# Performance work log

Hardware: AMD Instinct MI355X
Metric: run time of the kernel (lower is better)

Reference implementation:

```python
import jax, jax.numpy as jnp
import numpy as np

B, S, DM, H, DK, R, THETA = 8, 2048, 512, 8, 64, 128, 10000.0
BLK = R          # key/query block size; window radius == block size
NB = S // BLK    # number of blocks
NEG = -1e30      # additive mask for invalid positions (fp32-safe)


def setup_inputs() -> dict:
    key = jax.random.key(0)
    ks = jax.random.split(key, 5)
    scale = 0.02
    hidden_states = jax.random.normal(ks[0], (B, S, DM), jnp.float32)
    Wq = jax.random.normal(ks[1], (DM, H * DK), jnp.float32) * scale
    Wk = jax.random.normal(ks[2], (DM, H * DK), jnp.float32) * scale
    Wv = jax.random.normal(ks[3], (DM, H * DK), jnp.float32) * scale
    Wo = jax.random.normal(ks[4], (H * DK, DM), jnp.float32) * scale
    position_ids = jnp.tile(jnp.arange(S, dtype=jnp.int64)[None, :], (B, 1))
    return {"hidden_states": hidden_states, "Wq": Wq, "Wk": Wk, "Wv": Wv,
            "Wo": Wo, "position_ids": position_ids}


def _apply_rope(q, k, position_ids):
    # q,k: [B,H,S,DK]; position_ids: [B,S]
    half = DK // 2
    inv_freq = 1.0 / (THETA ** (jnp.arange(0, DK, 2, dtype=jnp.float32) / DK))  # [half]
    freqs = position_ids.astype(jnp.float32)[:, :, None] * inv_freq[None, None, :]  # [B,S,half]
    emb = jnp.concatenate([freqs, freqs], axis=-1)        # [B,S,DK]
    cos = jnp.cos(emb)[:, None, :, :]                     # [B,1,S,DK]
    sin = jnp.sin(emb)[:, None, :, :]

    def rotate_half(x):
        return jnp.concatenate([-x[..., half:], x[..., :half]], axis=-1)

    return q * cos + rotate_half(q) * sin, k * cos + rotate_half(k) * sin


def _band_mask():
    # valid[nb, BLK, 3*BLK]: key within [0,S) and |j - i| <= R
    b = jnp.arange(NB)[:, None, None]
    qi = jnp.arange(BLK)[None, :, None]
    kj = jnp.arange(3 * BLK)[None, None, :]
    kglob = (b - 1) * BLK + kj                 # global key index
    qglob = b * BLK + qi                        # global query index
    return (jnp.abs(kglob - qglob) <= R) & (kglob >= 0) & (kglob < S)


def reference(hidden_states, Wq, Wk, Wv, Wo, position_ids):
    # projections: [B,S,DM] -> [B,H,S,DK]
    def shape(x):
        return x.reshape(B, S, H, DK).transpose(0, 2, 1, 3)

    q = shape(hidden_states @ Wq)
    k = shape(hidden_states @ Wk)
    v = shape(hidden_states @ Wv)
    q, k = _apply_rope(q, k, position_ids)

    # block-banded sliding-window attention, softmax_scale = 1.0 (no scaling)
    pad = ((0, 0), (0, 0), (BLK, BLK), (0, 0))
    kb = jnp.pad(k, pad).reshape(B, H, NB + 2, BLK, DK)
    vb = jnp.pad(v, pad).reshape(B, H, NB + 2, BLK, DK)
    # neighbor window: blocks [b-1, b, b+1] -> [B,H,NB,3*BLK,DK]
    kwin = jnp.concatenate([kb[:, :, i:i + NB] for i in range(3)], axis=3)
    vwin = jnp.concatenate([vb[:, :, i:i + NB] for i in range(3)], axis=3)
    qb = q.reshape(B, H, NB, BLK, DK)

    scores = jnp.einsum('bhnqd,bhnkd->bhnqk', qb, kwin)   # unscaled
    valid = _band_mask()                                  # [NB,BLK,3*BLK]
    scores = jnp.where(valid[None, None], scores, NEG)
    attn = jax.nn.softmax(scores.astype(jnp.float32), axis=-1).astype(scores.dtype)
    outb = jnp.einsum('bhnqk,bhnkd->bhnqd', attn, vwin)   # [B,H,NB,BLK,DK]

    out = outb.reshape(B, H, S, DK).transpose(0, 2, 1, 3).reshape(B, S, H * DK)
    return out @ Wo
```

## Files before the change

kernel.cpp:

```cpp
#include <hip/hip_runtime.h>

using bf16 = __bf16;
typedef __bf16 bf16x8 __attribute__((ext_vector_type(8)));
typedef __bf16 bf16x4 __attribute__((ext_vector_type(4)));
typedef float f32x4 __attribute__((ext_vector_type(4)));
typedef float f32x16 __attribute__((ext_vector_type(16)));

#define MFMA16(a, b, c) __builtin_amdgcn_mfma_f32_16x16x32_bf16((a), (b), (c), 0, 0, 0)
#define MFMA32(a, b, c) __builtin_amdgcn_mfma_f32_32x32x16_bf16((a), (b), (c), 0, 0, 0)

constexpr int S = 2048, DM = 512, H = 8, DK = 64, HD = 512;
constexpr int NBLK = 16, BLK = 128;
constexpr int Mrows = 8 * S;
constexpr float LOG2E = 1.44269504088896340736f;

__device__ __forceinline__ void gll16(const void* g, void* l) {
  __builtin_amdgcn_global_load_lds((const __attribute__((address_space(1))) unsigned int*)g,
                                   (__attribute__((address_space(3))) unsigned int*)l, 16, 0, 0);
}

__global__ void k_conv(const float* __restrict__ x, bf16* __restrict__ y) {
  size_t i = ((size_t)blockIdx.x * 256 + threadIdx.x) * 8;
  float4 a = *(const float4*)(x + i);
  float4 b = *(const float4*)(x + i + 4);
  bf16x8 o;
  o[0] = (bf16)a.x; o[1] = (bf16)a.y; o[2] = (bf16)a.z; o[3] = (bf16)a.w;
  o[4] = (bf16)b.x; o[5] = (bf16)b.y; o[6] = (bf16)b.z; o[7] = (bf16)b.w;
  *(bf16x8*)(y + i) = o;
}

__global__ void k_transw4(const float* __restrict__ W0, const float* __restrict__ W1,
                          const float* __restrict__ W2, const float* __restrict__ W3,
                          bf16* __restrict__ D0, bf16* __restrict__ D1,
                          bf16* __restrict__ D2, bf16* __restrict__ D3) {
  const int z = blockIdx.z;
  const float* W = (z == 0) ? W0 : (z == 1) ? W1 : (z == 2) ? W2 : W3;
  bf16* Wt = (z == 0) ? D0 : (z == 1) ? D1 : (z == 2) ? D2 : D3;
  __shared__ float tile[32][33];
  int k0 = blockIdx.x * 32, n0 = blockIdx.y * 32;
  int tx = threadIdx.x, ty = threadIdx.y;
#pragma unroll
  for (int i = 0; i < 4; i++)
    tile[ty * 4 + i][tx] = W[(size_t)(k0 + ty * 4 + i) * 512 + n0 + tx];
  __syncthreads();
#pragma unroll
  for (int i = 0; i < 4; i++)
    Wt[(size_t)(n0 + ty * 4 + i) * 512 + k0 + tx] = (bf16)tile[tx][ty * 4 + i];
}

__global__ void k_ctab(float2* __restrict__ ctab) {
  int idx = blockIdx.x * 256 + threadIdx.x;
  int s = idx >> 5, i = idx & 31;
  float invf = exp2f(-(float)i * (13.287712379549449f / 32.0f));
  float ang = (float)s * invf;
  ctab[idx] = make_float2(cosf(ang), sinf(ang));
}

__global__ __launch_bounds__(256) void k_gemm_qkv(
    const bf16* __restrict__ Xb,
    const bf16* __restrict__ Wtq, const bf16* __restrict__ Wtk, const bf16* __restrict__ Wtv,
    bf16* __restrict__ Qo, bf16* __restrict__ Ko, bf16* __restrict__ Vt,
    const float2* __restrict__ ctab) {
  const int bid = blockIdx.x;
  const int xcd = bid & 7, i = bid >> 3;
  const int mloc = i / 12, zy = i % 12;
  const int z = zy >> 2, y = zy & 3;
  const bf16* Wt = (z == 0) ? Wtq : ((z == 1) ? Wtk : Wtv);
  bf16* dst = (z == 0) ? Qo : Ko;
  const float qscale = (z == 0) ? LOG2E : 1.0f;

  __shared__ __align__(16) char Asm2[2][8192];
  __shared__ __align__(16) char Bsm2[2][8192];

  const int t = threadIdx.x, l = t & 63, wid = t >> 6;
  const int l15 = l & 15, l4 = l >> 4;
  const int wm = wid >> 1, wn = wid & 1;
  const size_t arow0 = (size_t)(xcd * 16 + mloc) * 128;
  const size_t brow0 = (size_t)y * 128;

  f32x4 acc[4][4] = {};
  const int rs = wid * 16 + (l >> 2);
  const int cs = (l & 3) ^ ((l >> 2) & 3);

  auto stage = [&](int kt, int b) {
    const int k0 = kt * 32;
    gll16(Xb + (arow0 + rs) * 512 + k0 + cs * 8,      Asm2[b] + wid * 1024);
    gll16(Xb + (arow0 + 64 + rs) * 512 + k0 + cs * 8, Asm2[b] + 4096 + wid * 1024);
    gll16(Wt + (brow0 + rs) * 512 + k0 + cs * 8,      Bsm2[b] + wid * 1024);
    gll16(Wt + (brow0 + 64 + rs) * 512 + k0 + cs * 8, Bsm2[b] + 4096 + wid * 1024);
  };

  stage(0, 0);
  asm volatile("s_waitcnt vmcnt(0)" ::: "memory");
  __builtin_amdgcn_s_barrier();

  int cur = 0;
  for (int kt = 0; kt < 16; ++kt) {
    if (kt < 15) stage(kt + 1, cur ^ 1);
    bf16x8 af[4], bfr[4];
#pragma unroll
    for (int mi = 0; mi < 4; mi++) {
      int row = wm * 64 + mi * 16 + l15;
      af[mi] = *(const bf16x8*)(Asm2[cur] + row * 64 + ((l4 ^ (row & 3)) * 16));
    }
#pragma unroll
    for (int ni = 0; ni < 4; ni++) {
      int row = wn * 64 + ni * 16 + l15;
      bfr[ni] = *(const bf16x8*)(Bsm2[cur] + row * 64 + ((l4 ^ (row & 3)) * 16));
    }
#pragma unroll
    for (int mi = 0; mi < 4; mi++)
#pragma unroll
      for (int ni = 0; ni < 4; ni++)
        acc[mi][ni] = MFMA16(af[mi], bfr[ni], acc[mi][ni]);
    if (kt < 15) {
      asm volatile("s_waitcnt vmcnt(0)" ::: "memory");
      __builtin_amdgcn_s_barrier();
    }
    cur ^= 1;
  }

  if (z == 2) {
    const int b = (int)(arow0 >> 11);
#pragma unroll
    for (int mi = 0; mi < 4; mi++) {
      int scol = (int)(arow0 & 2047) + wm * 64 + mi * 16 + l4 * 4;
#pragma unroll
      for (int ni = 0; ni < 4; ni++) {
        int col = (int)brow0 + wn * 64 + ni * 16 + l15;
        int hh = col >> 6, dd = col & 63;
        bf16x4 pk = {(bf16)acc[mi][ni][0], (bf16)acc[mi][ni][1],
                     (bf16)acc[mi][ni][2], (bf16)acc[mi][ni][3]};
        *(bf16x4*)(Vt + ((size_t)((b * H + hh) * 64 + dd)) * 2048 + scol) = pk;
      }
    }
    return;
  }

#pragma unroll
  for (int mi = 0; mi < 4; mi++) {
#pragma unroll
    for (int r = 0; r < 4; r++) {
      int grow = (int)arow0 + wm * 64 + mi * 16 + l4 * 4 + r;
      size_t rowoff = (size_t)grow * 512 + brow0 + wn * 64;
      int s = grow & (S - 1);
      float2 cs0 = ctab[s * 32 + l15];
      float2 cs1 = ctab[s * 32 + 16 + l15];
#pragma unroll
      for (int ni = 0; ni < 4; ni++) {
        float a = acc[mi][ni][r];
        float b = acc[mi][ni ^ 2][r];
        float2 cc = (ni & 1) ? cs1 : cs0;
        float val = (ni < 2) ? (a * cc.x - b * cc.y) : (a * cc.x + b * cc.y);
        dst[rowoff + ni * 16 + l15] = (bf16)(val * qscale);
      }
    }
  }
}

__global__ __launch_bounds__(256) void k_gemm_out(
    const bf16* __restrict__ A, const bf16* __restrict__ Wt, float* __restrict__ out) {
  const int bid = blockIdx.x;
  const int xcd = bid & 7, i = bid >> 3;
  __shared__ __align__(16) char Asm2[2][8192];
  __shared__ __align__(16) char Bsm2[2][8192];

  const int t = threadIdx.x, l = t & 63, wid = t >> 6;
  const int l15 = l & 15, l4 = l >> 4;
  const int wm = wid >> 1, wn = wid & 1;
  const size_t arow0 = (size_t)(xcd * 16 + (i >> 2)) * 128;
  const size_t brow0 = (size_t)(i & 3) * 128;

  f32x4 acc[4][4] = {};
  const int rs = wid * 16 + (l >> 2);
  const int cs = (l & 3) ^ ((l >> 2) & 3);

  auto stage = [&](int kt, int b) {
    const int k0 = kt * 32;
    gll16(A + (arow0 + rs) * 512 + k0 + cs * 8,       Asm2[b] + wid * 1024);
    gll16(A + (arow0 + 64 + rs) * 512 + k0 + cs * 8,  Asm2[b] + 4096 + wid * 1024);
    gll16(Wt + (brow0 + rs) * 512 + k0 + cs * 8,      Bsm2[b] + wid * 1024);
    gll16(Wt + (brow0 + 64 + rs) * 512 + k0 + cs * 8, Bsm2[b] + 4096 + wid * 1024);
  };

  stage(0, 0);
  asm volatile("s_waitcnt vmcnt(0)" ::: "memory");
  __builtin_amdgcn_s_barrier();

  int cur = 0;
  for (int kt = 0; kt < 16; ++kt) {
    if (kt < 15) stage(kt + 1, cur ^ 1);
    bf16x8 af[4], bfr[4];
#pragma unroll
    for (int mi = 0; mi < 4; mi++) {
      int row = wm * 64 + mi * 16 + l15;
      af[mi] = *(const bf16x8*)(Asm2[cur] + row * 64 + ((l4 ^ (row & 3)) * 16));
    }
#pragma unroll
    for (int ni = 0; ni < 4; ni++) {
      int row = wn * 64 + ni * 16 + l15;
      bfr[ni] = *(const bf16x8*)(Bsm2[cur] + row * 64 + ((l4 ^ (row & 3)) * 16));
    }
#pragma unroll
    for (int mi = 0; mi < 4; mi++)
#pragma unroll
      for (int ni = 0; ni < 4; ni++)
        acc[mi][ni] = MFMA16(af[mi], bfr[ni], acc[mi][ni]);
    if (kt < 15) {
      asm volatile("s_waitcnt vmcnt(0)" ::: "memory");
      __builtin_amdgcn_s_barrier();
    }
    cur ^= 1;
  }

#pragma unroll
  for (int mi = 0; mi < 4; mi++)
#pragma unroll
    for (int r = 0; r < 4; r++) {
      int grow = (int)arow0 + wm * 64 + mi * 16 + l4 * 4 + r;
      size_t rowoff = (size_t)grow * 512 + brow0 + wn * 64;
#pragma unroll
      for (int ni = 0; ni < 4; ni++)
        out[rowoff + ni * 16 + l15] = acc[mi][ni][r];
    }
}

__global__ __launch_bounds__(256, 4) void k_attn(
    const bf16* __restrict__ Q, const bf16* __restrict__ K, const bf16* __restrict__ Vt,
    bf16* __restrict__ O) {
  const int bid = blockIdx.x;
  const int swz = (bid & 7) * 128 + (bid >> 3);
  const int nb = swz & 15, h = (swz >> 4) & 7, bb = swz >> 7;
  const int t = threadIdx.x, l = t & 63, w = t >> 6;
  const int q31 = l & 31, hi = l >> 5;

  const int bh = bb * H + h;
  const size_t qrow = (size_t)bb * S + nb * BLK + w * 32 + q31;

  const bf16* Qp = Q + qrow * HD + h * DK + hi * 8;
  bf16x8 qb[4];
#pragma unroll
  for (int ks = 0; ks < 4; ks++) qb[ks] = *(const bf16x8*)(Qp + ks * 16);

  f32x16 o0 = {}, o1 = {};
  float mrun = -3e38f, lrun = 0.f;

  const bf16* Kbase = K + (size_t)bb * S * HD + h * DK + hi * 8;
  const bf16* Vbase = Vt + ((size_t)bh * 64 + q31) * 2048 + hi * 8;
  const int s0 = nb * BLK + w * 32 - 128;

  auto pv = [&](const f32x16& p, int kgc) {
    unsigned int Wd[4][2];
#pragma unroll
    for (int a = 0; a < 4; a++)
#pragma unroll
      for (int b2 = 0; b2 < 2; b2++) {
        unsigned int wd;
        asm("v_cvt_pk_bf16_f32 %0, %1, %2" : "=v"(wd) : "v"(p[4 * a + 2 * b2]), "v"(p[4 * a + 2 * b2 + 1]));
        Wd[a][b2] = wd;
      }
    bf16x8 pf[2];
#pragma unroll
    for (int ks = 0; ks < 2; ks++) {
      union { unsigned int u[4]; bf16x8 v; } cvt;
#pragma unroll
      for (int b2 = 0; b2 < 2; b2++) {
        unsigned int low_w = Wd[2 * ks][b2];
        unsigned int hi_w  = Wd[2 * ks + 1][b2];
        unsigned int msg = hi ? low_w : hi_w;
        unsigned int rec = __shfl_xor(msg, 32);
        cvt.u[b2]     = hi ? rec : low_w;
        cvt.u[2 + b2] = hi ? hi_w : rec;
      }
      pf[ks] = cvt.v;
    }
    const bf16* Vp = Vbase + kgc;
    o0 = MFMA32(*(const bf16x8*)(Vp), pf[0], o0);
    o0 = MFMA32(*(const bf16x8*)(Vp + 16), pf[1], o0);
    o1 = MFMA32(*(const bf16x8*)(Vp + 32 * 2048), pf[0], o1);
    o1 = MFMA32(*(const bf16x8*)(Vp + 32 * 2048 + 16), pf[1], o1);
  };

#pragma unroll
  for (int st = 0; st < 5; ++st) {
    const bool has2 = (st < 4);
    const int c0 = st * 2, c1 = c0 + 1;
    const int kg0 = s0 + c0 * 32, kg1 = s0 + c1 * 32;
    const int kc0 = kg0 < 0 ? 0 : (kg0 > S - 32 ? S - 32 : kg0);
    const int kc1 = kg1 < 0 ? 0 : (kg1 > S - 32 ? S - 32 : kg1);

    f32x16 a0 = {}, a1 = {};
    {
      const bf16* Kp = Kbase + (size_t)(kc0 + q31) * HD;
      a0 = MFMA32(*(const bf16x8*)(Kp),      qb[0], a0);
      a0 = MFMA32(*(const bf16x8*)(Kp + 16), qb[1], a0);
      a0 = MFMA32(*(const bf16x8*)(Kp + 32), qb[2], a0);
      a0 = MFMA32(*(const bf16x8*)(Kp + 48), qb[3], a0);
    }
    if (has2) {
      const bf16* Kp = Kbase + (size_t)(kc1 + q31) * HD;
      a1 = MFMA32(*(const bf16x8*)(Kp),      qb[0], a1);
      a1 = MFMA32(*(const bf16x8*)(Kp + 16), qb[1], a1);
      a1 = MFMA32(*(const bf16x8*)(Kp + 32), qb[2], a1);
      a1 = MFMA32(*(const bf16x8*)(Kp + 48), qb[3], a1);
    }

    if (kg0 != kc0) {
#pragma unroll
      for (int rg = 0; rg < 16; rg++) a0[rg] = -1e30f;
    } else if (c0 == 0) {
#pragma unroll
      for (int rg = 0; rg < 16; rg++) {
        int kk = (rg & 3) + 8 * (rg >> 2) + 4 * hi;
        if (kk < q31) a0[rg] = -1e30f;
      }
    } else if (c0 == 8) {
#pragma unroll
      for (int rg = 0; rg < 16; rg++) {
        int kk = (rg & 3) + 8 * (rg >> 2) + 4 * hi;
        if (kk > q31) a0[rg] = -1e30f;
      }
    }
    if (has2 && kg1 != kc1) {
#pragma unroll
      for (int rg = 0; rg < 16; rg++) a1[rg] = -1e30f;
    }

    f32x16 mx = a0;
    if (has2) {
#pragma unroll
      for (int rg = 0; rg < 16; rg++) mx[rg] = fmaxf(mx[rg], a1[rg]);
    }
#pragma unroll
    for (int sl = 8; sl >= 1; sl >>= 1)
#pragma unroll
      for (int i2 = 0; i2 < sl; i2++) mx[i2] = fmaxf(mx[i2], mx[i2 + sl]);
    const float pm = fmaxf(mx[0], __shfl_xor(mx[0], 32));

    if (!__all(pm - mrun <= 8.0f)) {
      const float mnew = fmaxf(mrun, pm);
      const float alpha = exp2f(mrun - mnew);
      lrun *= alpha;
#pragma unroll
      for (int rg = 0; rg < 16; rg++) { o0[rg] *= alpha; o1[rg] *= alpha; }
      mrun = mnew;
    }

    float rsum = 0.f;
#pragma unroll
    for (int rg = 0; rg < 16; rg++) { a0[rg] = exp2f(a0[rg] - mrun); rsum += a0[rg]; }
    if (has2) {
#pragma unroll
      for (int rg = 0; rg < 16; rg++) { a1[rg] = exp2f(a1[rg] - mrun); rsum += a1[rg]; }
    }
    rsum += __shfl_xor(rsum, 32);
    lrun += rsum;

    pv(a0, kc0);
    if (has2) pv(a1, kc1);
  }

  const float inv = 1.0f / lrun;
  bf16* Op = O + qrow * HD + h * DK + 4 * hi;
#pragma unroll
  for (int dt = 0; dt < 2; dt++) {
    const f32x16 oo = dt ? o1 : o0;
#pragma unroll
    for (int a = 0; a < 4; a++) {
      bf16x4 ob = {(bf16)(oo[4 * a + 0] * inv), (bf16)(oo[4 * a + 1] * inv),
                   (bf16)(oo[4 * a + 2] * inv), (bf16)(oo[4 * a + 3] * inv)};
      *(bf16x4*)(Op + dt * 32 + 8 * a) = ob;
    }
  }
}

extern "C" void kernel_launch(void* const* d_in, const int* in_sizes, int n_in,
                              void* d_out, int out_size, void* d_ws, size_t ws_size,
                              hipStream_t stream) {
  const float* hs = (const float*)d_in[0];
  const float* Wq = (const float*)d_in[1];
  const float* Wk = (const float*)d_in[2];
  const float* Wv = (const float*)d_in[3];
  const float* Wo = (const float*)d_in[4];
  float* out = (float*)d_out;

  char* ws = (char*)d_ws;
  const size_t MB = 1u << 20;
  bf16* Xb = (bf16*)(ws);
  bf16* Qb = (bf16*)(ws + 16 * MB);
  bf16* Kb = (bf16*)(ws + 32 * MB);
  bf16* Vt = (bf16*)(ws + 48 * MB);
  bf16* Wtq = (bf16*)(ws + 64 * MB);
  bf16* Wtk = Wtq + 512 * 512;
  bf16* Wtv = Wtk + 512 * 512;
  bf16* Wto = Wtv + 512 * 512;
  float2* ctab = (float2*)(ws + 64 * MB + 4 * 512 * 512 * sizeof(bf16));
  bf16* AO = Xb;

  k_conv<<<dim3(Mrows * DM / (256 * 8)), dim3(256), 0, stream>>>(hs, Xb);
  k_transw4<<<dim3(16, 16, 4), dim3(32, 8), 0, stream>>>(Wq, Wk, Wv, Wo, Wtq, Wtk, Wtv, Wto);
  k_ctab<<<dim3(S * 32 / 256), dim3(256), 0, stream>>>(ctab);
  k_gemm_qkv<<<dim3(1536), dim3(256), 0, stream>>>(Xb, Wtq, Wtk, Wtv, Qb, Kb, Vt, ctab);
  k_attn<<<dim3(NBLK * H * 8), dim3(256), 0, stream>>>(Qb, Kb, Vt, AO);
  k_gemm_out<<<dim3(512), dim3(256), 0, stream>>>(AO, Wto, out);
}
```

Baseline: 124.7 us.

## Software-pipeline K/V loads across single 32-key chunks in attention loop

Measured after the change: 126.1 us. About the same (+1.1%).

```diff
diff --git a/kernel.cpp b/kernel.cpp
--- a/kernel.cpp
+++ b/kernel.cpp
@@ -249,15 +249,88 @@
   const bf16* Vbase = Vt + ((size_t)bh * 64 + q31) * 2048 + hi * 8;
   const int s0 = nb * BLK + w * 32 - 128;
 
-  auto pv = [&](const f32x16& p, int kgc) {
+  auto kcl = [](int kg) { return kg < 0 ? 0 : (kg > S - 32 ? S - 32 : kg); };
+
+  bf16x8 kcur0, kcur1, kcur2, kcur3;
+  {
+    const bf16* Kp = Kbase + (size_t)(kcl(s0) + q31) * HD;
+    kcur0 = *(const bf16x8*)(Kp);
+    kcur1 = *(const bf16x8*)(Kp + 16);
+    kcur2 = *(const bf16x8*)(Kp + 32);
+    kcur3 = *(const bf16x8*)(Kp + 48);
+  }
+
+#pragma unroll
+  for (int c = 0; c < 9; ++c) {
+    const int kg = s0 + c * 32;
+    const int kcc = kcl(kg);
+    const int kcn = kcl(s0 + (c + 1) * 32);
+
+    const bf16* Vp = Vbase + kcc;
+    bf16x8 v0 = *(const bf16x8*)(Vp);
+    bf16x8 v1 = *(const bf16x8*)(Vp + 16);
+    bf16x8 v2 = *(const bf16x8*)(Vp + 32 * 2048);
+    bf16x8 v3 = *(const bf16x8*)(Vp + 32 * 2048 + 16);
+    const bf16* Kpn = Kbase + (size_t)(kcn + q31) * HD;
+    bf16x8 kn0 = *(const bf16x8*)(Kpn);
+    bf16x8 kn1 = *(const bf16x8*)(Kpn + 16);
+    bf16x8 kn2 = *(const bf16x8*)(Kpn + 32);
+    bf16x8 kn3 = *(const bf16x8*)(Kpn + 48);
+    __builtin_amdgcn_sched_barrier(0);
+
+    f32x16 a = {};
+    a = MFMA32(kcur0, qb[0], a);
+    a = MFMA32(kcur1, qb[1], a);
+    a = MFMA32(kcur2, qb[2], a);
+    a = MFMA32(kcur3, qb[3], a);
+
+    if (kg != kcc) {
+#pragma unroll
+      for (int rg = 0; rg < 16; rg++) a[rg] = -1e30f;
+    } else if (c == 0) {
+#pragma unroll
+      for (int rg = 0; rg < 16; rg++) {
+        int kk = (rg & 3) + 8 * (rg >> 2) + 4 * hi;
+        if (kk < q31) a[rg] = -1e30f;
+      }
+    } else if (c == 8) {
+#pragma unroll
+      for (int rg = 0; rg < 16; rg++) {
+        int kk = (rg & 3) + 8 * (rg >> 2) + 4 * hi;
+        if (kk > q31) a[rg] = -1e30f;
+      }
+    }
+
+    f32x16 mx = a;
+#pragma unroll
+    for (int sl = 8; sl >= 1; sl >>= 1)
+#pragma unroll
+      for (int i2 = 0; i2 < sl; i2++) mx[i2] = fmaxf(mx[i2], mx[i2 + sl]);
+    const float pm = fmaxf(mx[0], __shfl_xor(mx[0], 32));
+
+    if (!__all(pm - mrun <= 8.0f)) {
+      const float mnew = fmaxf(mrun, pm);
+      const float alpha = exp2f(mrun - mnew);
+      lrun *= alpha;
+#pragma unroll
+      for (int rg = 0; rg < 16; rg++) { o0[rg] *= alpha; o1[rg] *= alpha; }
+      mrun = mnew;
+    }
+
+    float rsum = 0.f;
+#pragma unroll
+    for (int rg = 0; rg < 16; rg++) { a[rg] = exp2f(a[rg] - mrun); rsum += a[rg]; }
+    rsum += __shfl_xor(rsum, 32);
+    lrun += rsum;
+
     unsigned int Wd[4][2];
 #pragma unroll
-    for (int a = 0; a < 4; a++)
+    for (int aa = 0; aa < 4; aa++)
 #pragma unroll
       for (int b2 = 0; b2 < 2; b2++) {
         unsigned int wd;
-        asm("v_cvt_pk_bf16_f32 %0, %1, %2" : "=v"(wd) : "v"(p[4 * a + 2 * b2]), "v"(p[4 * a + 2 * b2 + 1]));
-        Wd[a][b2] = wd;
+        asm("v_cvt_pk_bf16_f32 %0, %1, %2" : "=v"(wd) : "v"(a[4 * aa + 2 * b2]), "v"(a[4 * aa + 2 * b2 + 1]));
+        Wd[aa][b2] = wd;
       }
     bf16x8 pf[2];
 #pragma unroll
@@ -274,90 +347,13 @@
       }
       pf[ks] = cvt.v;
     }
-    const bf16* Vp = Vbase + kgc;
-    o0 = MFMA32(*(const bf16x8*)(Vp), pf[0], o0);
-    o0 = MFMA32(*(const bf16x8*)(Vp + 16), pf[1], o0);
-    o1 = MFMA32(*(const bf16x8*)(Vp + 32 * 2048), pf[0], o1);
-    o1 = MFMA32(*(const bf16x8*)(Vp + 32 * 2048 + 16), pf[1], o1);
-  };
-
-#pragma unroll
-  for (int st = 0; st < 5; ++st) {
-    const bool has2 = (st < 4);
-    const int c0 = st * 2, c1 = c0 + 1;
-    const int kg0 = s0 + c0 * 32, kg1 = s0 + c1 * 32;
-    const int kc0 = kg0 < 0 ? 0 : (kg0 > S - 32 ? S - 32 : kg0);
-    const int kc1 = kg1 < 0 ? 0 : (kg1 > S - 32 ? S - 32 : kg1);
-
-    f32x16 a0 = {}, a1 = {};
-    {
-      const bf16* Kp = Kbase + (size_t)(kc0 + q31) * HD;
-      a0 = MFMA32(*(const bf16x8*)(Kp),      qb[0], a0);
-      a0 = MFMA32(*(const bf16x8*)(Kp + 16), qb[1], a0);
-      a0 = MFMA32(*(const bf16x8*)(Kp + 32), qb[2], a0);
-      a0 = MFMA32(*(const bf16x8*)(Kp + 48), qb[3], a0);
-    }
-    if (has2) {
-      const bf16* Kp = Kbase + (size_t)(kc1 + q31) * HD;
-      a1 = MFMA32(*(const bf16x8*)(Kp),      qb[0], a1);
-      a1 = MFMA32(*(const bf16x8*)(Kp + 16), qb[1], a1);
-      a1 = MFMA32(*(const bf16x8*)(Kp + 32), qb[2], a1);
-      a1 = MFMA32(*(const bf16x8*)(Kp + 48), qb[3], a1);
-    }
-
-    if (kg0 != kc0) {
-#pragma unroll
-      for (int rg = 0; rg < 16; rg++) a0[rg] = -1e30f;
-    } else if (c0 == 0) {
-#pragma unroll
-      for (int rg = 0; rg < 16; rg++) {
-        int kk = (rg & 3) + 8 * (rg >> 2) + 4 * hi;
-        if (kk < q31) a0[rg] = -1e30f;
-      }
-    } else if (c0 == 8) {
-#pragma unroll
-      for (int rg = 0; rg < 16; rg++) {
-        int kk = (rg & 3) + 8 * (rg >> 2) + 4 * hi;
-        if (kk > q31) a0[rg] = -1e30f;
-      }
-    }
-    if (has2 && kg1 != kc1) {
-#pragma unroll
-      for (int rg = 0; rg < 16; rg++) a1[rg] = -1e30f;
-    }
-
-    f32x16 mx = a0;
-    if (has2) {
-#pragma unroll
-      for (int rg = 0; rg < 16; rg++) mx[rg] = fmaxf(mx[rg], a1[rg]);
-    }
-#pragma unroll
-    for (int sl = 8; sl >= 1; sl >>= 1)
-#pragma unroll
-      for (int i2 = 0; i2 < sl; i2++) mx[i2] = fmaxf(mx[i2], mx[i2 + sl]);
-    const float pm = fmaxf(mx[0], __shfl_xor(mx[0], 32));
-
-    if (!__all(pm - mrun <= 8.0f)) {
-      const float mnew = fmaxf(mrun, pm);
-      const float alpha = exp2f(mrun - mnew);
-      lrun *= alpha;
-#pragma unroll
-      for (int rg = 0; rg < 16; rg++) { o0[rg] *= alpha; o1[rg] *= alpha; }
-      mrun = mnew;
-    }
-
-    float rsum = 0.f;
-#pragma unroll
-    for (int rg = 0; rg < 16; rg++) { a0[rg] = exp2f(a0[rg] - mrun); rsum += a0[rg]; }
-    if (has2) {
-#pragma unroll
-      for (int rg = 0; rg < 16; rg++) { a1[rg] = exp2f(a1[rg] - mrun); rsum += a1[rg]; }
-    }
-    rsum += __shfl_xor(rsum, 32);
-    lrun += rsum;
-
-    pv(a0, kc0);
-    if (has2) pv(a1, kc1);
+
+    o0 = MFMA32(v0, pf[0], o0);
+    o0 = MFMA32(v1, pf[1], o0);
+    o1 = MFMA32(v2, pf[0], o1);
+    o1 = MFMA32(v3, pf[1], o1);
+
+    kcur0 = kn0; kcur1 = kn1; kcur2 = kn2; kcur3 = kn3;
   }
 
   const float inv = 1.0f / lrun;
@@ -366,10 +362,10 @@
   for (int dt = 0; dt < 2; dt++) {
     const f32x16 oo = dt ? o1 : o0;
 #pragma unroll
-    for (int a = 0; a < 4; a++) {
-      bf16x4 ob = {(bf16)(oo[4 * a + 0] * inv), (bf16)(oo[4 * a + 1] * inv),
-                   (bf16)(oo[4 * a + 2] * inv), (bf16)(oo[4 * a + 3] * inv)};
-      *(bf16x4*)(Op + dt * 32 + 8 * a) = ob;
+    for (int a2 = 0; a2 < 4; a2++) {
+      bf16x4 ob = {(bf16)(oo[4 * a2 + 0] * inv), (bf16)(oo[4 * a2 + 1] * inv),
+                   (bf16)(oo[4 * a2 + 2] * inv), (bf16)(oo[4 * a2 + 3] * inv)};
+      *(bf16x4*)(Op + dt * 32 + 8 * a2) = ob;
     }
   }
 }
```

## Triple-buffer GEMM LDS staging, change swizzle, and raise wave priority around attention MFMAs

Applied to the files above, without the earlier changes.

New measurement: 119.8 us. 3.9% less time.

```diff
diff --git a/kernel.cpp b/kernel.cpp
--- a/kernel.cpp
+++ b/kernel.cpp
@@ -69,8 +69,8 @@
   bf16* dst = (z == 0) ? Qo : Ko;
   const float qscale = (z == 0) ? LOG2E : 1.0f;
 
-  __shared__ __align__(16) char Asm2[2][8192];
-  __shared__ __align__(16) char Bsm2[2][8192];
+  __shared__ __align__(16) char Asm3[3][8192];
+  __shared__ __align__(16) char Bsm3[3][8192];
 
   const int t = threadIdx.x, l = t & 63, wid = t >> 6;
   const int l15 = l & 15, l4 = l >> 4;
@@ -80,33 +80,34 @@
 
   f32x4 acc[4][4] = {};
   const int rs = wid * 16 + (l >> 2);
-  const int cs = (l & 3) ^ ((l >> 2) & 3);
+  const int cs = (l & 3) ^ (l >> 4);
 
   auto stage = [&](int kt, int b) {
     const int k0 = kt * 32;
-    gll16(Xb + (arow0 + rs) * 512 + k0 + cs * 8,      Asm2[b] + wid * 1024);
-    gll16(Xb + (arow0 + 64 + rs) * 512 + k0 + cs * 8, Asm2[b] + 4096 + wid * 1024);
-    gll16(Wt + (brow0 + rs) * 512 + k0 + cs * 8,      Bsm2[b] + wid * 1024);
-    gll16(Wt + (brow0 + 64 + rs) * 512 + k0 + cs * 8, Bsm2[b] + 4096 + wid * 1024);
+    gll16(Xb + (arow0 + rs) * 512 + k0 + cs * 8,      Asm3[b] + wid * 1024);
+    gll16(Xb + (arow0 + 64 + rs) * 512 + k0 + cs * 8, Asm3[b] + 4096 + wid * 1024);
+    gll16(Wt + (brow0 + rs) * 512 + k0 + cs * 8,      Bsm3[b] + wid * 1024);
+    gll16(Wt + (brow0 + 64 + rs) * 512 + k0 + cs * 8, Bsm3[b] + 4096 + wid * 1024);
   };
 
   stage(0, 0);
-  asm volatile("s_waitcnt vmcnt(0)" ::: "memory");
+  stage(1, 1);
+  asm volatile("s_waitcnt vmcnt(4)" ::: "memory");
   __builtin_amdgcn_s_barrier();
 
   int cur = 0;
   for (int kt = 0; kt < 16; ++kt) {
-    if (kt < 15) stage(kt + 1, cur ^ 1);
+    if (kt + 2 <= 15) stage(kt + 2, (kt + 2) % 3);
     bf16x8 af[4], bfr[4];
 #pragma unroll
     for (int mi = 0; mi < 4; mi++) {
       int row = wm * 64 + mi * 16 + l15;
-      af[mi] = *(const bf16x8*)(Asm2[cur] + row * 64 + ((l4 ^ (row & 3)) * 16));
+      af[mi] = *(const bf16x8*)(Asm3[cur] + row * 64 + ((l4 ^ (l15 >> 2)) * 16));
     }
 #pragma unroll
     for (int ni = 0; ni < 4; ni++) {
       int row = wn * 64 + ni * 16 + l15;
-      bfr[ni] = *(const bf16x8*)(Bsm2[cur] + row * 64 + ((l4 ^ (row & 3)) * 16));
+      bfr[ni] = *(const bf16x8*)(Bsm3[cur] + row * 64 + ((l4 ^ (l15 >> 2)) * 16));
     }
 #pragma unroll
     for (int mi = 0; mi < 4; mi++)
@@ -114,10 +115,11 @@
       for (int ni = 0; ni < 4; ni++)
         acc[mi][ni] = MFMA16(af[mi], bfr[ni], acc[mi][ni]);
     if (kt < 15) {
-      asm volatile("s_waitcnt vmcnt(0)" ::: "memory");
+      if (kt < 14) asm volatile("s_waitcnt vmcnt(4)" ::: "memory");
+      else         asm volatile("s_waitcnt vmcnt(0)" ::: "memory");
       __builtin_amdgcn_s_barrier();
     }
-    cur ^= 1;
+    cur = (cur == 2) ? 0 : cur + 1;
   }
 
   if (z == 2) {
@@ -162,8 +164,8 @@
     const bf16* __restrict__ A, const bf16* __restrict__ Wt, float* __restrict__ out) {
   const int bid = blockIdx.x;
   const int xcd = bid & 7, i = bid >> 3;
-  __shared__ __align__(16) char Asm2[2][8192];
-  __shared__ __align__(16) char Bsm2[2][8192];
+  __shared__ __align__(16) char Asm3[3][8192];
+  __shared__ __align__(16) char Bsm3[3][8192];
 
   const int t = threadIdx.x, l = t & 63, wid = t >> 6;
   const int l15 = l & 15, l4 = l >> 4;
@@ -173,33 +175,34 @@
 
   f32x4 acc[4][4] = {};
   const int rs = wid * 16 + (l >> 2);
-  const int cs = (l & 3) ^ ((l >> 2) & 3);
+  const int cs = (l & 3) ^ (l >> 4);
 
   auto stage = [&](int kt, int b) {
     const int k0 = kt * 32;
-    gll16(A + (arow0 + rs) * 512 + k0 + cs * 8,       Asm2[b] + wid * 1024);
-    gll16(A + (arow0 + 64 + rs) * 512 + k0 + cs * 8,  Asm2[b] + 4096 + wid * 1024);
-    gll16(Wt + (brow0 + rs) * 512 + k0 + cs * 8,      Bsm2[b] + wid * 1024);
-    gll16(Wt + (brow0 + 64 + rs) * 512 + k0 + cs * 8, Bsm2[b] + 4096 + wid * 1024);
+    gll16(A + (arow0 + rs) * 512 + k0 + cs * 8,       Asm3[b] + wid * 1024);
+    gll16(A + (arow0 + 64 + rs) * 512 + k0 + cs * 8,  Asm3[b] + 4096 + wid * 1024);
+    gll16(Wt + (brow0 + rs) * 512 + k0 + cs * 8,      Bsm3[b] + wid * 1024);
+    gll16(Wt + (brow0 + 64 + rs) * 512 + k0 + cs * 8, Bsm3[b] + 4096 + wid * 1024);
   };
 
   stage(0, 0);
-  asm volatile("s_waitcnt vmcnt(0)" ::: "memory");
+  stage(1, 1);
+  asm volatile("s_waitcnt vmcnt(4)" ::: "memory");
   __builtin_amdgcn_s_barrier();
 
   int cur = 0;
   for (int kt = 0; kt < 16; ++kt) {
-    if (kt < 15) stage(kt + 1, cur ^ 1);
+    if (kt + 2 <= 15) stage(kt + 2, (kt + 2) % 3);
     bf16x8 af[4], bfr[4];
 #pragma unroll
     for (int mi = 0; mi < 4; mi++) {
       int row = wm * 64 + mi * 16 + l15;
-      af[mi] = *(const bf16x8*)(Asm2[cur] + row * 64 + ((l4 ^ (row & 3)) * 16));
+      af[mi] = *(const bf16x8*)(Asm3[cur] + row * 64 + ((l4 ^ (l15 >> 2)) * 16));
     }
 #pragma unroll
     for (int ni = 0; ni < 4; ni++) {
       int row = wn * 64 + ni * 16 + l15;
-      bfr[ni] = *(const bf16x8*)(Bsm2[cur] + row * 64 + ((l4 ^ (row & 3)) * 16));
+      bfr[ni] = *(const bf16x8*)(Bsm3[cur] + row * 64 + ((l4 ^ (l15 >> 2)) * 16));
     }
 #pragma unroll
     for (int mi = 0; mi < 4; mi++)
@@ -207,10 +210,11 @@
       for (int ni = 0; ni < 4; ni++)
         acc[mi][ni] = MFMA16(af[mi], bfr[ni], acc[mi][ni]);
     if (kt < 15) {
-      asm volatile("s_waitcnt vmcnt(0)" ::: "memory");
+      if (kt < 14) asm volatile("s_waitcnt vmcnt(4)" ::: "memory");
+      else         asm volatile("s_waitcnt vmcnt(0)" ::: "memory");
       __builtin_amdgcn_s_barrier();
     }
-    cur ^= 1;
+    cur = (cur == 2) ? 0 : cur + 1;
   }
 
 #pragma unroll
@@ -275,10 +279,12 @@
       pf[ks] = cvt.v;
     }
     const bf16* Vp = Vbase + kgc;
+    __builtin_amdgcn_s_setprio(1);
     o0 = MFMA32(*(const bf16x8*)(Vp), pf[0], o0);
     o0 = MFMA32(*(const bf16x8*)(Vp + 16), pf[1], o0);
     o1 = MFMA32(*(const bf16x8*)(Vp + 32 * 2048), pf[0], o1);
     o1 = MFMA32(*(const bf16x8*)(Vp + 32 * 2048 + 16), pf[1], o1);
+    __builtin_amdgcn_s_setprio(0);
   };
 
 #pragma unroll
@@ -292,17 +298,21 @@
     f32x16 a0 = {}, a1 = {};
     {
       const bf16* Kp = Kbase + (size_t)(kc0 + q31) * HD;
+      __builtin_amdgcn_s_setprio(1);
       a0 = MFMA32(*(const bf16x8*)(Kp),      qb[0], a0);
       a0 = MFMA32(*(const bf16x8*)(Kp + 16), qb[1], a0);
       a0 = MFMA32(*(const bf16x8*)(Kp + 32), qb[2], a0);
       a0 = MFMA32(*(const bf16x8*)(Kp + 48), qb[3], a0);
+      __builtin_amdgcn_s_setprio(0);
     }
     if (has2) {
       const bf16* Kp = Kbase + (size_t)(kc1 + q31) * HD;
+      __builtin_amdgcn_s_setprio(1);
       a1 = MFMA32(*(const bf16x8*)(Kp),      qb[0], a1);
       a1 = MFMA32(*(const bf16x8*)(Kp + 16), qb[1], a1);
       a1 = MFMA32(*(const bf16x8*)(Kp + 32), qb[2], a1);
       a1 = MFMA32(*(const bf16x8*)(Kp + 48), qb[3], a1);
+      __builtin_amdgcn_s_setprio(0);
     }
 
     if (kg0 != kc0) {
```
